# Kernel tuning notes

Measured on AMD Instinct MI355X. Metric: run time of the kernel, lower is better.

The kernel has to match this reference:

```python
import jax, jax.numpy as jnp
import numpy as np

EMBED = 1024
HEADS = 16


def setup_inputs() -> dict:
    key = jax.random.key(0)
    k1, k2, k3 = jax.random.split(key, 3)
    B, S, D = 2, 2048, EMBED
    x = jax.random.normal(k1, (B, S, D), dtype=jnp.float32)
    # nn.Linear weights: stored as [out, in]; y = x @ W.T
    w_qkv = jax.random.normal(k2, (3 * D, D), dtype=jnp.float32) * (D ** -0.5)
    w_out = jax.random.normal(k3, (D, D), dtype=jnp.float32) * (D ** -0.5)
    return {"x": x, "w_qkv": w_qkv, "w_out": w_out}


def reference(x, w_qkv, w_out):
    B, S, D = x.shape
    H = HEADS
    hd = D // H
    qkv = x @ w_qkv.T                       # [B, S, 3D]
    q, k, v = jnp.split(qkv, 3, axis=-1)
    # 'b l (head k) -> b head l k'
    def heads(t):
        return t.reshape(B, S, H, hd).transpose(0, 2, 1, 3)
    q, k, v = heads(q), heads(k), heads(v)
    scale = hd ** 0.5
    scores = jnp.einsum('bhqd,bhkd->bhqk', q, k) / scale
    probs = jax.nn.softmax(scores, axis=-1)
    out = jnp.einsum('bhqk,bhkd->bhqd', probs, v)  # [B, H, S, hd]
    out = out.transpose(0, 2, 1, 3).reshape(B, S, D)
    return out @ w_out.T
```

## Files before the change

### kernel.cpp

```cpp
#include <hip/hip_runtime.h>

typedef short short8 __attribute__((ext_vector_type(8)));
typedef short short4v __attribute__((ext_vector_type(4)));
typedef float floatx4 __attribute__((ext_vector_type(4)));
typedef unsigned short ushort_t;

#define EMBED 1024
#define HEADS 16
#define HD 64
#define SEQ 2048
#define BATCH 2
#define QSCALE 0.18033688f

__device__ inline ushort_t f2bf(float f) {
    unsigned int u = __float_as_uint(f);
    u += 0x7fff + ((u >> 16) & 1);
    return (ushort_t)(u >> 16);
}

typedef const __attribute__((address_space(1))) unsigned int* gas_t;
typedef __attribute__((address_space(3))) unsigned int* las_t;
__device__ inline void async_copy16(const ushort_t* g, ushort_t* l) {
    __builtin_amdgcn_global_load_lds((gas_t)g, (las_t)l, 16, 0, 0);
}

__global__ void cast3_kernel(const float* __restrict__ a, ushort_t* __restrict__ oa, int na,
                             const float* __restrict__ b, ushort_t* __restrict__ ob, int nb,
                             const float* __restrict__ c, ushort_t* __restrict__ oc, int nc) {
    int idx = (blockIdx.x * blockDim.x + threadIdx.x) * 4;
    const float* in; ushort_t* out;
    if (idx < na)            { in = a;  out = oa; }
    else if (idx < na + nb)  { in = b;  out = ob; idx -= na; }
    else if (idx < na + nb + nc) { in = c; out = oc; idx -= na + nb; }
    else return;
    float4 f = *(const float4*)(in + idx);
    ushort4 o;
    o.x = f2bf(f.x); o.y = f2bf(f.y); o.z = f2bf(f.z); o.w = f2bf(f.w);
    *(ushort4*)(out + idx) = o;
}

#define BM 128
#define BK 64

template<int MODE, int TBN>
__launch_bounds__(256, 3)
__global__ void gemm_bt(const ushort_t* __restrict__ A, const ushort_t* __restrict__ B,
                        float* __restrict__ outF,
                        ushort_t* __restrict__ qb, ushort_t* __restrict__ kb,
                        ushort_t* __restrict__ vtb,
                        int M, int N, int K) {
    __shared__ ushort_t As[BM * BK];
    __shared__ ushort_t Bs[TBN * BK];
    const int id   = blockIdx.x;
    const int jj   = id >> 3;
    const int bm   = (id & 7) * 4 + (jj & 3);
    const int bn   = jj >> 2;
    const int t    = threadIdx.x;
    const int lane = t & 63;
    const int wave = t >> 6;
    const int wm   = (wave >> 1) * 64;
    const int wn   = (wave & 1) * (TBN / 2);
    const int m0   = bm * BM;
    const int n0   = bn * TBN;
    const int col  = lane & 15;
    const int quad = lane >> 4;
    constexpr int NJ = TBN / 32;

    const int srow = lane >> 3;
    const int sgr  = (lane & 7) ^ (srow & 7);
    const int slot0 = quad ^ (col & 7);

    floatx4 acc[4][NJ] = {};

    for (int k0 = 0; k0 < K; k0 += BK) {
        for (int half = 0; half < 4; ++half) {
            int row0 = wave * 32 + half * 8;
            int r = row0 + srow;
            async_copy16(A + (size_t)(m0 + r) * K + k0 + sgr * 8, &As[row0 * BK]);
        }
        for (int half = 0; half < TBN / 32; ++half) {
            int row0 = wave * (TBN / 4) + half * 8;
            int r = row0 + srow;
            async_copy16(B + (size_t)(n0 + r) * K + k0 + sgr * 8, &Bs[row0 * BK]);
        }
        __syncthreads();
        short8 a[2][4], b[2][NJ];
        for (int i = 0; i < 4; ++i) {
            int base = (wm + i * 16 + col) * BK;
            a[0][i] = *(const short8*)(&As[base + slot0 * 8]);
            a[1][i] = *(const short8*)(&As[base + (slot0 ^ 4) * 8]);
        }
        for (int j = 0; j < NJ; ++j) {
            int base = (wn + j * 16 + col) * BK;
            b[0][j] = *(const short8*)(&Bs[base + slot0 * 8]);
            b[1][j] = *(const short8*)(&Bs[base + (slot0 ^ 4) * 8]);
        }
        for (int kk = 0; kk < 2; ++kk)
            for (int i = 0; i < 4; ++i)
                for (int j = 0; j < NJ; ++j)
                    acc[i][j] = __builtin_amdgcn_mfma_f32_16x16x32_bf16(a[kk][i], b[kk][j], acc[i][j], 0, 0, 0);
        __syncthreads();
    }

    for (int i = 0; i < 4; ++i)
        for (int j = 0; j < NJ; ++j) {
            int n = n0 + wn + j * 16 + col;
            int mb = m0 + wm + i * 16 + quad * 4;
            if (MODE == 1) {
                for (int r = 0; r < 4; ++r)
                    outF[(size_t)(mb + r) * N + n] = acc[i][j][r];
            } else {
                int part = n >> 10;
                int within = n & 1023;
                int h = within >> 6, d = within & 63;
                int bb = mb >> 11, s = mb & 2047;
                if (part == 2) {
                    short4v pv;
                    pv.x = (short)f2bf(acc[i][j][0]); pv.y = (short)f2bf(acc[i][j][1]);
                    pv.z = (short)f2bf(acc[i][j][2]); pv.w = (short)f2bf(acc[i][j][3]);
                    *(short4v*)(vtb + (((size_t)bb * HEADS + h) * HD + d) * SEQ + s) = pv;
                } else {
                    ushort_t* dst = (part == 0) ? qb : kb;
                    const float scl = (part == 0) ? QSCALE : 1.0f;
                    for (int r = 0; r < 4; ++r)
                        dst[(((size_t)bb * HEADS + h) * SEQ + s + r) * HD + d] = f2bf(acc[i][j][r] * scl);
                }
            }
        }
}

__launch_bounds__(512, 4)
__global__ void attn_kernel(const ushort_t* __restrict__ qb_, const ushort_t* __restrict__ kb,
                            const ushort_t* __restrict__ vtb, ushort_t* __restrict__ attn) {
    __shared__ __align__(16) ushort_t lds[32768];
    const int id   = blockIdx.x;
    const int jj   = id >> 3;
    const int bh   = (id & 7) * 4 + (jj >> 4);
    const int qblk = jj & 15;
    const int t    = threadIdx.x;
    const int lane = t & 63;
    const int wave = t >> 6;
    const int g    = wave >> 2;
    const int wv   = wave & 3;
    const int col  = lane & 15;
    const int quad = lane >> 4;
    const int q0   = qblk * 128 + wv * 32;
    const int srow = lane >> 3;
    const int sgr  = lane & 7;

    auto swz = [](int r) { return (r & 7) ^ ((r >> 1) & 4) ^ ((r >> 3) & 2); };

    const ushort_t* Q  = qb_ + (size_t)bh * SEQ * HD;
    const ushort_t* Kp = kb  + (size_t)bh * SEQ * HD;
    const ushort_t* Vt = vtb + (size_t)bh * HD * SEQ;

    ushort_t* Kb0 = &lds[g * 8192];
    ushort_t* Vb0 = &lds[16384 + g * 8192];

    auto stage = [&](int c, int buf) {
        int kt = c << 6;
        #pragma unroll
        for (int inst = 0; inst < 2; ++inst) {
            int row0 = wv * 16 + inst * 8;
            int r = row0 + srow;
            int gr = sgr ^ swz(r);
            async_copy16(Kp + (size_t)(kt + r) * HD + gr * 8,
                         Kb0 + buf * 4096 + row0 * 64);
            async_copy16(Vt + (size_t)r * SEQ + kt + gr * 8,
                         Vb0 + buf * 4096 + row0 * 64);
        }
    };

    short8 qf[2][2];
    #pragma unroll
    for (int qt = 0; qt < 2; ++qt) {
        qf[qt][0] = *(const short8*)(Q + (size_t)(q0 + qt * 16 + col) * HD + quad * 8);
        qf[qt][1] = *(const short8*)(Q + (size_t)(q0 + qt * 16 + col) * HD + 32 + quad * 8);
    }

    const short8 ones8 = { (short)0x3F80, (short)0x3F80, (short)0x3F80, (short)0x3F80,
                           (short)0x3F80, (short)0x3F80, (short)0x3F80, (short)0x3F80 };

    floatx4 acc[2][4] = {};
    floatx4 accl[2] = {};

    stage(g, 0);
    __syncthreads();

    for (int i = 0; i < 16; ++i) {
        const int cur = i & 1;
        if (i < 15) stage(2 * (i + 1) + g, cur ^ 1);
        const ushort_t* Kc = Kb0 + cur * 4096;
        const ushort_t* Vc = Vb0 + cur * 4096;

        #pragma unroll
        for (int h = 0; h < 2; ++h) {
            short8 kf[2][2], vf8[4];
            #pragma unroll
            for (int nl = 0; nl < 2; ++nl) {
                int krow = h * 32 + ((col >> 2) << 3) + (col & 3) + nl * 4;
                int sk = swz(krow);
                kf[nl][0] = *(const short8*)(Kc + krow * 64 + ((quad ^ sk) * 8));
                kf[nl][1] = *(const short8*)(Kc + krow * 64 + (((4 + quad) ^ sk) * 8));
            }
            #pragma unroll
            for (int dt = 0; dt < 4; ++dt) {
                int vrow = dt * 16 + col;
                vf8[dt] = *(const short8*)(Vc + vrow * 64 + (((h * 4 + quad) ^ swz(vrow)) * 8));
            }
            #pragma unroll
            for (int qt = 0; qt < 2; ++qt) {
                unsigned pk[4];
                #pragma unroll
                for (int nl = 0; nl < 2; ++nl) {
                    floatx4 z = {};
                    __builtin_amdgcn_s_setprio(1);
                    z = __builtin_amdgcn_mfma_f32_16x16x32_bf16(kf[nl][0], qf[qt][0], z, 0, 0, 0);
                    z = __builtin_amdgcn_mfma_f32_16x16x32_bf16(kf[nl][1], qf[qt][1], z, 0, 0, 0);
                    __builtin_amdgcn_s_setprio(0);
                    unsigned u0 = __float_as_uint(__builtin_amdgcn_exp2f(z[0]));
                    unsigned u1 = __float_as_uint(__builtin_amdgcn_exp2f(z[1]));
                    unsigned u2 = __float_as_uint(__builtin_amdgcn_exp2f(z[2]));
                    unsigned u3 = __float_as_uint(__builtin_amdgcn_exp2f(z[3]));
                    pk[nl * 2 + 0] = __builtin_amdgcn_perm(u1, u0, 0x07060302u);
                    pk[nl * 2 + 1] = __builtin_amdgcn_perm(u3, u2, 0x07060302u);
                }
                short8 pb8 = *(short8*)pk;
                __builtin_amdgcn_s_setprio(1);
                accl[qt] = __builtin_amdgcn_mfma_f32_16x16x32_bf16(
                    ones8, pb8, accl[qt], 0, 0, 0);
                #pragma unroll
                for (int dt = 0; dt < 4; ++dt)
                    acc[qt][dt] = __builtin_amdgcn_mfma_f32_16x16x32_bf16(
                        vf8[dt], pb8, acc[qt][dt], 0, 0, 0);
                __builtin_amdgcn_s_setprio(0);
            }
        }
        __syncthreads();
    }

    float lsum[2] = { accl[0][0], accl[1][0] };

    float* fs = (float*)lds;
    const int slot = (wave * 64 + lane) * 20;
    floatx4 accK[4];
    float lsK;
    if (g == 0) {
        #pragma unroll
        for (int d = 0; d < 4; ++d) { *(floatx4*)(&fs[slot + d * 4]) = acc[1][d]; accK[d] = acc[0][d]; }
        fs[slot + 16] = lsum[1]; lsK = lsum[0];
    } else {
        #pragma unroll
        for (int d = 0; d < 4; ++d) { *(floatx4*)(&fs[slot + d * 4]) = acc[0][d]; accK[d] = acc[1][d]; }
        fs[slot + 16] = lsum[0]; lsK = lsum[1];
    }
    __syncthreads();
    const int pslot = ((wave ^ 4) * 64 + lane) * 20;
    #pragma unroll
    for (int d = 0; d < 4; ++d)
        accK[d] += *(const floatx4*)(&fs[pslot + d * 4]);
    float s = lsK + fs[pslot + 16];
    float inv = 1.0f / s;

    int b = bh >> 4, hh = bh & 15;
    int row = q0 + g * 16 + col;
    #pragma unroll
    for (int dt = 0; dt < 4; ++dt) {
        short4v o;
        o.x = (short)f2bf(accK[dt][0] * inv);
        o.y = (short)f2bf(accK[dt][1] * inv);
        o.z = (short)f2bf(accK[dt][2] * inv);
        o.w = (short)f2bf(accK[dt][3] * inv);
        *(short4v*)(attn + ((size_t)b * SEQ + row) * EMBED + hh * HD + dt * 16 + quad * 4) = o;
    }
}

extern "C" void kernel_launch(void* const* d_in, const int* in_sizes, int n_in,
                              void* d_out, int out_size, void* d_ws, size_t ws_size,
                              hipStream_t stream) {
    const float* x     = (const float*)d_in[0];
    const float* w_qkv = (const float*)d_in[1];
    const float* w_out = (const float*)d_in[2];
    float* out = (float*)d_out;

    char* ws = (char*)d_ws;
    size_t off = 0;
    ushort_t* x_bf    = (ushort_t*)(ws + off); off += (size_t)BATCH * SEQ * EMBED * 2;
    ushort_t* wqkv_bf = (ushort_t*)(ws + off); off += (size_t)3 * EMBED * EMBED * 2;
    ushort_t* wout_bf = (ushort_t*)(ws + off); off += (size_t)EMBED * EMBED * 2;
    ushort_t* q_buf   = (ushort_t*)(ws + off); off += (size_t)BATCH * HEADS * SEQ * HD * 2;
    ushort_t* k_buf   = (ushort_t*)(ws + off); off += (size_t)BATCH * HEADS * SEQ * HD * 2;
    ushort_t* vt_buf  = (ushort_t*)(ws + off); off += (size_t)BATCH * HEADS * SEQ * HD * 2;
    ushort_t* attn_bf = (ushort_t*)(ws + off); off += (size_t)BATCH * SEQ * EMBED * 2;

    int n_x = BATCH * SEQ * EMBED, n_wq = 3 * EMBED * EMBED, n_wo = EMBED * EMBED;
    int n_all = n_x + n_wq + n_wo;
    cast3_kernel<<<n_all / 1024, 256, 0, stream>>>(x, x_bf, n_x, w_qkv, wqkv_bf, n_wq,
                                                   w_out, wout_bf, n_wo);

    gemm_bt<0, 128><<<768, 256, 0, stream>>>(
        x_bf, wqkv_bf, nullptr, q_buf, k_buf, vt_buf, BATCH * SEQ, 3 * EMBED, EMBED);

    attn_kernel<<<512, 512, 0, stream>>>(q_buf, k_buf, vt_buf, attn_bf);

    gemm_bt<1, 64><<<512, 256, 0, stream>>>(
        attn_bf, wout_bf, out, nullptr, nullptr, nullptr, BATCH * SEQ, EMBED, EMBED);
}
```

Baseline: 162.2 us.

## Double attention query tile per block to halve K/V reloads

Each attention block now handles 256 query rows instead of 128, with each wave computing four 16-row query tiles against every staged K/V chunk, and the grid shrinks from 512 to 256 blocks. This halves global K/V traffic and LDS staging per query and amortizes the K/V fragment reads over more MFMAs. In exchange it raises register pressure (launch bounds relaxed to 2 blocks/CU), lowers occupancy and block count (256 blocks on 256 CUs), and does the cross-group reduction in two LDS rounds with extra barriers. The kernel's softmax has no max subtraction, and that is unchanged.

```diff
diff --git a/kernel.cpp b/kernel.cpp
--- a/kernel.cpp
+++ b/kernel.cpp
@@ -129,14 +129,14 @@
         }
 }
 
-__launch_bounds__(512, 4)
+__launch_bounds__(512, 2)
 __global__ void attn_kernel(const ushort_t* __restrict__ qb_, const ushort_t* __restrict__ kb,
                             const ushort_t* __restrict__ vtb, ushort_t* __restrict__ attn) {
     __shared__ __align__(16) ushort_t lds[32768];
     const int id   = blockIdx.x;
     const int jj   = id >> 3;
-    const int bh   = (id & 7) * 4 + (jj >> 4);
-    const int qblk = jj & 15;
+    const int bh   = (id & 7) * 4 + (jj >> 3);
+    const int qblk = jj & 7;
     const int t    = threadIdx.x;
     const int lane = t & 63;
     const int wave = t >> 6;
@@ -144,7 +144,7 @@
     const int wv   = wave & 3;
     const int col  = lane & 15;
     const int quad = lane >> 4;
-    const int q0   = qblk * 128 + wv * 32;
+    const int q0   = qblk * 256 + wv * 64;
     const int srow = lane >> 3;
     const int sgr  = lane & 7;
 
@@ -171,9 +171,9 @@
         }
     };
 
-    short8 qf[2][2];
+    short8 qf[4][2];
     #pragma unroll
-    for (int qt = 0; qt < 2; ++qt) {
+    for (int qt = 0; qt < 4; ++qt) {
         qf[qt][0] = *(const short8*)(Q + (size_t)(q0 + qt * 16 + col) * HD + quad * 8);
         qf[qt][1] = *(const short8*)(Q + (size_t)(q0 + qt * 16 + col) * HD + 32 + quad * 8);
     }
@@ -181,8 +181,8 @@
     const short8 ones8 = { (short)0x3F80, (short)0x3F80, (short)0x3F80, (short)0x3F80,
                            (short)0x3F80, (short)0x3F80, (short)0x3F80, (short)0x3F80 };
 
-    floatx4 acc[2][4] = {};
-    floatx4 accl[2] = {};
+    floatx4 acc[4][4] = {};
+    floatx4 accl[4] = {};
 
     stage(g, 0);
     __syncthreads();
@@ -209,7 +209,7 @@
                 vf8[dt] = *(const short8*)(Vc + vrow * 64 + (((h * 4 + quad) ^ swz(vrow)) * 8));
             }
             #pragma unroll
-            for (int qt = 0; qt < 2; ++qt) {
+            for (int qt = 0; qt < 4; ++qt) {
                 unsigned pk[4];
                 #pragma unroll
                 for (int nl = 0; nl < 2; ++nl) {
@@ -239,39 +239,41 @@
         __syncthreads();
     }
 
-    float lsum[2] = { accl[0][0], accl[1][0] };
-
     float* fs = (float*)lds;
-    const int slot = (wave * 64 + lane) * 20;
-    floatx4 accK[4];
-    float lsK;
-    if (g == 0) {
-        #pragma unroll
-        for (int d = 0; d < 4; ++d) { *(floatx4*)(&fs[slot + d * 4]) = acc[1][d]; accK[d] = acc[0][d]; }
-        fs[slot + 16] = lsum[1]; lsK = lsum[0];
-    } else {
-        #pragma unroll
-        for (int d = 0; d < 4; ++d) { *(floatx4*)(&fs[slot + d * 4]) = acc[0][d]; accK[d] = acc[1][d]; }
-        fs[slot + 16] = lsum[0]; lsK = lsum[1];
-    }
-    __syncthreads();
+    const int slot  = (wave * 64 + lane) * 20;
     const int pslot = ((wave ^ 4) * 64 + lane) * 20;
+    floatx4 accK[2][4];
+    float lsK[2];
     #pragma unroll
-    for (int d = 0; d < 4; ++d)
-        accK[d] += *(const floatx4*)(&fs[pslot + d * 4]);
-    float s = lsK + fs[pslot + 16];
-    float inv = 1.0f / s;
+    for (int r2 = 0; r2 < 2; ++r2) {
+        const int sendqt = (g == 0) ? 2 + r2 : r2;
+        const int keepqt = 2 * g + r2;
+        #pragma unroll
+        for (int d = 0; d < 4; ++d)
+            *(floatx4*)(&fs[slot + d * 4]) = acc[sendqt][d];
+        fs[slot + 16] = accl[sendqt][0];
+        __syncthreads();
+        #pragma unroll
+        for (int d = 0; d < 4; ++d)
+            accK[r2][d] = acc[keepqt][d] + *(const floatx4*)(&fs[pslot + d * 4]);
+        lsK[r2] = accl[keepqt][0] + fs[pslot + 16];
+        __syncthreads();
+    }
 
     int b = bh >> 4, hh = bh & 15;
-    int row = q0 + g * 16 + col;
     #pragma unroll
-    for (int dt = 0; dt < 4; ++dt) {
-        short4v o;
-        o.x = (short)f2bf(accK[dt][0] * inv);
-        o.y = (short)f2bf(accK[dt][1] * inv);
-        o.z = (short)f2bf(accK[dt][2] * inv);
-        o.w = (short)f2bf(accK[dt][3] * inv);
-        *(short4v*)(attn + ((size_t)b * SEQ + row) * EMBED + hh * HD + dt * 16 + quad * 4) = o;
+    for (int r2 = 0; r2 < 2; ++r2) {
+        float inv = 1.0f / lsK[r2];
+        int row = q0 + (2 * g + r2) * 16 + col;
+        #pragma unroll
+        for (int dt = 0; dt < 4; ++dt) {
+            short4v o;
+            o.x = (short)f2bf(accK[r2][dt][0] * inv);
+            o.y = (short)f2bf(accK[r2][dt][1] * inv);
+            o.z = (short)f2bf(accK[r2][dt][2] * inv);
+            o.w = (short)f2bf(accK[r2][dt][3] * inv);
+            *(short4v*)(attn + ((size_t)b * SEQ + row) * EMBED + hh * HD + dt * 16 + quad * 4) = o;
+        }
     }
 }
 
@@ -301,7 +303,7 @@
     gemm_bt<0, 128><<<768, 256, 0, stream>>>(
         x_bf, wqkv_bf, nullptr, q_buf, k_buf, vt_buf, BATCH * SEQ, 3 * EMBED, EMBED);
 
-    attn_kernel<<<512, 512, 0, stream>>>(q_buf, k_buf, vt_buf, attn_bf);
+    attn_kernel<<<256, 512, 0, stream>>>(q_buf, k_buf, vt_buf, attn_bf);
 
     gemm_bt<1, 64><<<512, 256, 0, stream>>>(
         attn_bf, wout_bf, out, nullptr, nullptr, nullptr, BATCH * SEQ, EMBED, EMBED);
```

Measured after the change: 383.9 us. +136.7%, slower.
